# Kernel optimization log

Hardware: AMD Instinct MI355X
Metric: run time of the kernel (lower is better)

Reference implementation:

```python
import jax, jax.numpy as jnp
import numpy as np

N_NODES = 50000

def setup_inputs() -> dict:
    key = jax.random.key(0)
    k1, k2, k3, k4, k5 = jax.random.split(key, 5)
    feat = jax.random.normal(k1, (N_NODES, 192), dtype=jnp.float32)
    edge_feat = jax.random.normal(k2, (800000, 64), dtype=jnp.float32)
    src = jax.random.randint(k3, (800000,), 0, N_NODES, dtype=jnp.int32)
    dst = jax.random.randint(k4, (800000,), 0, N_NODES, dtype=jnp.int32)
    weight = jax.random.normal(k5, (256, 256), dtype=jnp.float32) * (1.0 / np.sqrt(256.0))
    bias = jnp.zeros((256,), dtype=jnp.float32)
    return {"feat": feat, "edge_feat": edge_feat, "src": src, "dst": dst,
            "weight": weight, "bias": bias}


def reference(feat, edge_feat, src, dst, weight, bias):
    N = feat.shape[0]
    ones_e = jnp.ones(src.shape[0], dtype=jnp.float32)
    # out-degree normalization of source features (pre-aggregation)
    out_deg = jnp.clip(jax.ops.segment_sum(ones_e, src, num_segments=N), 1.0, None)
    feat_n = feat * (out_deg ** -0.5)[:, None]            # [N, d_node]
    # message = concat(src_feat_norm, edge_feat); sum over dst.
    # segment_sum distributes over concat, so aggregate parts separately
    # (avoids materializing the [E, d_node+d_edge] message tensor).
    h_src = jax.ops.segment_sum(feat_n[src], dst, num_segments=N)   # [N, d_node]
    h_edge = jax.ops.segment_sum(edge_feat, dst, num_segments=N)    # [N, d_edge]
    h = jnp.concatenate([h_src, h_edge], axis=1)          # [N, in_feats]
    rst = h @ weight                                      # [N, out_feats]
    # in-degree normalization (post-aggregation)
    in_deg = jnp.clip(jax.ops.segment_sum(ones_e, dst, num_segments=N), 1.0, None)
    rst = rst * (in_deg ** -0.5)[:, None] + bias
    return rst
```

## Files before the change

kernel.cpp:

```cpp
#include <hip/hip_runtime.h>

#define NN 50000
#define NE 800000
#define DIN 256
#define DOUT 256


__global__ __launch_bounds__(256) void zero_meta(int* __restrict__ p, int n) {
    int i = blockIdx.x * 256 + threadIdx.x;
    if (i < n) p[i] = 0;
}

__global__ __launch_bounds__(256) void count_kernel(const int* __restrict__ src,
                                                    const int* __restrict__ dst,
                                                    int* __restrict__ in_cnt,
                                                    int* __restrict__ out_cnt) {
    int e = blockIdx.x * 256 + threadIdx.x;
    if (e < NE) {
        atomicAdd(in_cnt + dst[e], 1);
        atomicAdd(out_cnt + src[e], 1);
    }
}

__global__ __launch_bounds__(256) void scan1(const int* __restrict__ cnt,
                                             int* __restrict__ row_off,
                                             int* __restrict__ bsum) {
    __shared__ int tmp[256];
    int tid = threadIdx.x;
    int i = blockIdx.x * 256 + tid;
    int v = (i < NN) ? cnt[i] : 0;
    tmp[tid] = v;
    __syncthreads();
#pragma unroll
    for (int off = 1; off < 256; off <<= 1) {
        int t = (tid >= off) ? tmp[tid - off] : 0;
        __syncthreads();
        if (tid >= off) tmp[tid] += t;
        __syncthreads();
    }
    if (i < NN) row_off[i] = tmp[tid] - v;
    if (tid == 255) bsum[blockIdx.x] = tmp[255];
}

__global__ __launch_bounds__(256) void scan2(int* __restrict__ bsum, int nb) {
    __shared__ int tmp[256];
    int tid = threadIdx.x;
    int v = (tid < nb) ? bsum[tid] : 0;
    tmp[tid] = v;
    __syncthreads();
#pragma unroll
    for (int off = 1; off < 256; off <<= 1) {
        int t = (tid >= off) ? tmp[tid - off] : 0;
        __syncthreads();
        if (tid >= off) tmp[tid] += t;
        __syncthreads();
    }
    if (tid < nb) bsum[tid] = tmp[tid] - v;
}

__global__ __launch_bounds__(256) void scan3(int* __restrict__ row_off,
                                             int* __restrict__ cursor,
                                             const int* __restrict__ bsum) {
    int i = blockIdx.x * 256 + threadIdx.x;
    if (i < NN) {
        int v = row_off[i] + bsum[i >> 8];
        row_off[i] = v;
        cursor[i] = v;
    }
    if (i == NN) row_off[NN] = NE;
}

__global__ __launch_bounds__(256) void norm_out(const int* __restrict__ out_cnt,
                                                float* __restrict__ odeg_inv) {
    int i = blockIdx.x * 256 + threadIdx.x;
    if (i < NN) odeg_inv[i] = rsqrtf((float)max(out_cnt[i], 1));
}

__global__ __launch_bounds__(256) void fill_kernel(const int* __restrict__ src,
                                                   const int* __restrict__ dst,
                                                   int* __restrict__ cursor,
                                                   int2* __restrict__ perm2) {
    int e = blockIdx.x * 256 + threadIdx.x;
    if (e < NE) {
        int d = dst[e];
        int pos = atomicAdd(cursor + d, 1);
        perm2[pos] = make_int2(e, src[e]);
    }
}

__global__ __launch_bounds__(256) void aggregate_kernel(const float* __restrict__ feat,
                                                        const float* __restrict__ edge_feat,
                                                        const int* __restrict__ row_off,
                                                        const float* __restrict__ odeg_inv,
                                                        const int2* __restrict__ perm2,
                                                        float* __restrict__ h) {
    int node = blockIdx.x * 4 + (threadIdx.x >> 6);
    int lane = threadIdx.x & 63;
    if (node >= NN) return;
    int start = row_off[node];
    int end   = row_off[node + 1];

    bool isF = lane < 48;
    const float* base = isF ? feat : edge_feat;
    int stride = isF ? 192 : 64;
    int loff   = isF ? lane * 4 : (lane - 48) * 4;

    float4 acc = make_float4(0.f, 0.f, 0.f, 0.f);
    int i = start;
    for (; i + 4 <= end; i += 4) {
        int2 p0 = perm2[i + 0];
        int2 p1 = perm2[i + 1];
        int2 p2 = perm2[i + 2];
        int2 p3 = perm2[i + 3];
        int i0 = isF ? p0.y : p0.x;
        int i1 = isF ? p1.y : p1.x;
        int i2 = isF ? p2.y : p2.x;
        int i3 = isF ? p3.y : p3.x;
        float4 v0 = *(const float4*)(base + (size_t)i0 * stride + loff);
        float4 v1 = *(const float4*)(base + (size_t)i1 * stride + loff);
        float4 v2 = *(const float4*)(base + (size_t)i2 * stride + loff);
        float4 v3 = *(const float4*)(base + (size_t)i3 * stride + loff);
        float s0 = odeg_inv[p0.y]; if (!isF) s0 = 1.f;
        float s1 = odeg_inv[p1.y]; if (!isF) s1 = 1.f;
        float s2 = odeg_inv[p2.y]; if (!isF) s2 = 1.f;
        float s3 = odeg_inv[p3.y]; if (!isF) s3 = 1.f;
        acc.x = fmaf(v0.x, s0, acc.x); acc.y = fmaf(v0.y, s0, acc.y);
        acc.z = fmaf(v0.z, s0, acc.z); acc.w = fmaf(v0.w, s0, acc.w);
        acc.x = fmaf(v1.x, s1, acc.x); acc.y = fmaf(v1.y, s1, acc.y);
        acc.z = fmaf(v1.z, s1, acc.z); acc.w = fmaf(v1.w, s1, acc.w);
        acc.x = fmaf(v2.x, s2, acc.x); acc.y = fmaf(v2.y, s2, acc.y);
        acc.z = fmaf(v2.z, s2, acc.z); acc.w = fmaf(v2.w, s2, acc.w);
        acc.x = fmaf(v3.x, s3, acc.x); acc.y = fmaf(v3.y, s3, acc.y);
        acc.z = fmaf(v3.z, s3, acc.z); acc.w = fmaf(v3.w, s3, acc.w);
    }
    for (; i < end; ++i) {
        int2 p = perm2[i];
        int idx = isF ? p.y : p.x;
        float4 v = *(const float4*)(base + (size_t)idx * stride + loff);
        float s = odeg_inv[p.y]; if (!isF) s = 1.f;
        acc.x = fmaf(v.x, s, acc.x); acc.y = fmaf(v.y, s, acc.y);
        acc.z = fmaf(v.z, s, acc.z); acc.w = fmaf(v.w, s, acc.w);
    }
    ((float4*)h)[(size_t)node * 64 + lane] = acc;
}

#define HPAD 260
__global__ __launch_bounds__(256) void gemm_kernel(const float* __restrict__ h,
                                                   const float* __restrict__ W,
                                                   const float* __restrict__ bias,
                                                   const int* __restrict__ row_off,
                                                   float* __restrict__ out) {
    __shared__ float hs[32 * HPAD];
    int block_row = blockIdx.x * 32;

    for (int i = threadIdx.x; i < 32 * 64; i += 256) {
        int r = i >> 6, c4 = i & 63;
        int row = block_row + r;
        float4 v = make_float4(0.f, 0.f, 0.f, 0.f);
        if (row < NN) v = ((const float4*)h)[(size_t)row * 64 + c4];
        *(float4*)&hs[r * HPAD + c4 * 4] = v;
    }
    __syncthreads();

    int cg = threadIdx.x & 31;
    int rg = threadIdx.x >> 5;

    float acc[4][8];
#pragma unroll
    for (int i = 0; i < 4; ++i)
#pragma unroll
        for (int j = 0; j < 8; ++j) acc[i][j] = 0.f;

    const float4* W4 = (const float4*)W;
    for (int k4 = 0; k4 < 64; ++k4) {
        float4 a[4];
#pragma unroll
        for (int i = 0; i < 4; ++i)
            a[i] = *(const float4*)&hs[(rg * 4 + i) * HPAD + k4 * 4];
#pragma unroll
        for (int kk = 0; kk < 4; ++kk) {
            int k = k4 * 4 + kk;
            float4 w0 = W4[k * 64 + cg * 2];
            float4 w1 = W4[k * 64 + cg * 2 + 1];
#pragma unroll
            for (int i = 0; i < 4; ++i) {
                float av = ((const float*)&a[i])[kk];
                acc[i][0] = fmaf(av, w0.x, acc[i][0]);
                acc[i][1] = fmaf(av, w0.y, acc[i][1]);
                acc[i][2] = fmaf(av, w0.z, acc[i][2]);
                acc[i][3] = fmaf(av, w0.w, acc[i][3]);
                acc[i][4] = fmaf(av, w1.x, acc[i][4]);
                acc[i][5] = fmaf(av, w1.y, acc[i][5]);
                acc[i][6] = fmaf(av, w1.z, acc[i][6]);
                acc[i][7] = fmaf(av, w1.w, acc[i][7]);
            }
        }
    }

    float4 b0 = ((const float4*)bias)[cg * 2];
    float4 b1 = ((const float4*)bias)[cg * 2 + 1];
#pragma unroll
    for (int i = 0; i < 4; ++i) {
        int row = block_row + rg * 4 + i;
        if (row < NN) {
            int deg = row_off[row + 1] - row_off[row];
            float s = rsqrtf((float)max(deg, 1));
            float4 o0 = make_float4(acc[i][0] * s + b0.x, acc[i][1] * s + b0.y,
                                    acc[i][2] * s + b0.z, acc[i][3] * s + b0.w);
            float4 o1 = make_float4(acc[i][4] * s + b1.x, acc[i][5] * s + b1.y,
                                    acc[i][6] * s + b1.z, acc[i][7] * s + b1.w);
            float4* op = (float4*)(out + (size_t)row * DOUT + cg * 8);
            op[0] = o0;
            op[1] = o1;
        }
    }
}

extern "C" void kernel_launch(void* const* d_in, const int* in_sizes, int n_in,
                              void* d_out, int out_size, void* d_ws, size_t ws_size,
                              hipStream_t stream) {
    const float* feat      = (const float*)d_in[0];
    const float* edge_feat = (const float*)d_in[1];
    const int*   src       = (const int*)d_in[2];
    const int*   dst       = (const int*)d_in[3];
    const float* W         = (const float*)d_in[4];
    const float* bias      = (const float*)d_in[5];
    float* out = (float*)d_out;

    float* h        = (float*)d_ws;
    int*   row_off  = (int*)(h + (size_t)NN * DIN);
    float* odeg_inv = (float*)(row_off + NN + 2);
    int*   cursor   = (int*)(odeg_inv + NN);
    int*   bsum     = cursor + NN;
    int2*  perm2    = (int2*)(bsum + 256);
    int*   in_cnt   = (int*)perm2;
    int*   out_cnt  = in_cnt + NN;

    const int SCAN_BLOCKS = (NN + 255) / 256;

    zero_meta<<<(2 * NN + 255) / 256, 256, 0, stream>>>(in_cnt, 2 * NN);

    count_kernel<<<(NE + 255) / 256, 256, 0, stream>>>(src, dst, in_cnt, out_cnt);

    scan1<<<SCAN_BLOCKS, 256, 0, stream>>>(in_cnt, row_off, bsum);
    scan2<<<1, 256, 0, stream>>>(bsum, SCAN_BLOCKS);
    scan3<<<(NN + 256) / 256, 256, 0, stream>>>(row_off, cursor, bsum);

    norm_out<<<(NN + 255) / 256, 256, 0, stream>>>(out_cnt, odeg_inv);

    fill_kernel<<<(NE + 255) / 256, 256, 0, stream>>>(src, dst, cursor, perm2);

    aggregate_kernel<<<(NN + 3) / 4, 256, 0, stream>>>(feat, edge_feat, row_off,
                                                       odeg_inv, perm2, h);

    gemm_kernel<<<(NN + 31) / 32, 256, 0, stream>>>(h, W, bias, row_off, out);
}
```

Baseline: 615.9 us.

## Use bf16 MFMA GEMM, store aggregated features as bf16, widen gather unroll

Replaces the fp32 FMA GEMM with a bf16 MFMA 16x16x32 GEMM that reads a pre-transposed bf16 copy of the weight, converted by a new wconv kernel. The aggregation kernel now writes bf16 instead of fp32, halving the intermediate traffic, and gathers 8 edges per iteration with a clamped, masked tail instead of a 4-way unroll plus remainder loop. The out-degree normalisation is folded into scan3, so one launch disappears. The cost is lower precision in h and W (bf16 rounding), plus an extra launch for the weight conversion.

```diff
diff --git a/kernel.cpp b/kernel.cpp
--- a/kernel.cpp
+++ b/kernel.cpp
@@ -4,6 +4,15 @@
 #define NE 800000
 #define DIN 256
 #define DOUT 256
+
+typedef __attribute__((ext_vector_type(8))) short bf16x8;
+typedef __attribute__((ext_vector_type(4))) float f32x4;
+
+__device__ __forceinline__ unsigned short f2bf(float x) {
+    unsigned int u = __builtin_bit_cast(unsigned int, x);
+    u += 0x7fffu + ((u >> 16) & 1u);
+    return (unsigned short)(u >> 16);
+}
 
 
 __global__ __launch_bounds__(256) void zero_meta(int* __restrict__ p, int n) {
@@ -60,20 +69,23 @@
 
 __global__ __launch_bounds__(256) void scan3(int* __restrict__ row_off,
                                              int* __restrict__ cursor,
+                                             float* __restrict__ odeg_inv,
+                                             const int* __restrict__ out_cnt,
                                              const int* __restrict__ bsum) {
     int i = blockIdx.x * 256 + threadIdx.x;
     if (i < NN) {
         int v = row_off[i] + bsum[i >> 8];
         row_off[i] = v;
         cursor[i] = v;
+        odeg_inv[i] = rsqrtf((float)max(out_cnt[i], 1));
     }
     if (i == NN) row_off[NN] = NE;
 }
 
-__global__ __launch_bounds__(256) void norm_out(const int* __restrict__ out_cnt,
-                                                float* __restrict__ odeg_inv) {
-    int i = blockIdx.x * 256 + threadIdx.x;
-    if (i < NN) odeg_inv[i] = rsqrtf((float)max(out_cnt[i], 1));
+__global__ __launch_bounds__(256) void wconv(const float* __restrict__ W,
+                                             unsigned short* __restrict__ wt) {
+    int n = blockIdx.x, k = threadIdx.x;
+    wt[n * 256 + k] = f2bf(W[k * 256 + n]);
 }
 
 __global__ __launch_bounds__(256) void fill_kernel(const int* __restrict__ src,
@@ -93,7 +105,7 @@
                                                         const int* __restrict__ row_off,
                                                         const float* __restrict__ odeg_inv,
                                                         const int2* __restrict__ perm2,
-                                                        float* __restrict__ h) {
+                                                        unsigned short* __restrict__ h_bf) {
     int node = blockIdx.x * 4 + (threadIdx.x >> 6);
     int lane = threadIdx.x & 63;
     if (node >= NN) return;
@@ -106,113 +118,97 @@
     int loff   = isF ? lane * 4 : (lane - 48) * 4;
 
     float4 acc = make_float4(0.f, 0.f, 0.f, 0.f);
-    int i = start;
-    for (; i + 4 <= end; i += 4) {
-        int2 p0 = perm2[i + 0];
-        int2 p1 = perm2[i + 1];
-        int2 p2 = perm2[i + 2];
-        int2 p3 = perm2[i + 3];
-        int i0 = isF ? p0.y : p0.x;
-        int i1 = isF ? p1.y : p1.x;
-        int i2 = isF ? p2.y : p2.x;
-        int i3 = isF ? p3.y : p3.x;
-        float4 v0 = *(const float4*)(base + (size_t)i0 * stride + loff);
-        float4 v1 = *(const float4*)(base + (size_t)i1 * stride + loff);
-        float4 v2 = *(const float4*)(base + (size_t)i2 * stride + loff);
-        float4 v3 = *(const float4*)(base + (size_t)i3 * stride + loff);
-        float s0 = odeg_inv[p0.y]; if (!isF) s0 = 1.f;
-        float s1 = odeg_inv[p1.y]; if (!isF) s1 = 1.f;
-        float s2 = odeg_inv[p2.y]; if (!isF) s2 = 1.f;
-        float s3 = odeg_inv[p3.y]; if (!isF) s3 = 1.f;
-        acc.x = fmaf(v0.x, s0, acc.x); acc.y = fmaf(v0.y, s0, acc.y);
-        acc.z = fmaf(v0.z, s0, acc.z); acc.w = fmaf(v0.w, s0, acc.w);
-        acc.x = fmaf(v1.x, s1, acc.x); acc.y = fmaf(v1.y, s1, acc.y);
-        acc.z = fmaf(v1.z, s1, acc.z); acc.w = fmaf(v1.w, s1, acc.w);
-        acc.x = fmaf(v2.x, s2, acc.x); acc.y = fmaf(v2.y, s2, acc.y);
-        acc.z = fmaf(v2.z, s2, acc.z); acc.w = fmaf(v2.w, s2, acc.w);
-        acc.x = fmaf(v3.x, s3, acc.x); acc.y = fmaf(v3.y, s3, acc.y);
-        acc.z = fmaf(v3.z, s3, acc.z); acc.w = fmaf(v3.w, s3, acc.w);
-    }
-    for (; i < end; ++i) {
-        int2 p = perm2[i];
-        int idx = isF ? p.y : p.x;
-        float4 v = *(const float4*)(base + (size_t)idx * stride + loff);
-        float s = odeg_inv[p.y]; if (!isF) s = 1.f;
-        acc.x = fmaf(v.x, s, acc.x); acc.y = fmaf(v.y, s, acc.y);
-        acc.z = fmaf(v.z, s, acc.z); acc.w = fmaf(v.w, s, acc.w);
-    }
-    ((float4*)h)[(size_t)node * 64 + lane] = acc;
-}
-
-#define HPAD 260
-__global__ __launch_bounds__(256) void gemm_kernel(const float* __restrict__ h,
-                                                   const float* __restrict__ W,
-                                                   const float* __restrict__ bias,
-                                                   const int* __restrict__ row_off,
-                                                   float* __restrict__ out) {
-    __shared__ float hs[32 * HPAD];
-    int block_row = blockIdx.x * 32;
-
-    for (int i = threadIdx.x; i < 32 * 64; i += 256) {
-        int r = i >> 6, c4 = i & 63;
-        int row = block_row + r;
-        float4 v = make_float4(0.f, 0.f, 0.f, 0.f);
-        if (row < NN) v = ((const float4*)h)[(size_t)row * 64 + c4];
-        *(float4*)&hs[r * HPAD + c4 * 4] = v;
-    }
-    __syncthreads();
-
-    int cg = threadIdx.x & 31;
-    int rg = threadIdx.x >> 5;
-
-    float acc[4][8];
-#pragma unroll
-    for (int i = 0; i < 4; ++i)
-#pragma unroll
-        for (int j = 0; j < 8; ++j) acc[i][j] = 0.f;
-
-    const float4* W4 = (const float4*)W;
-    for (int k4 = 0; k4 < 64; ++k4) {
-        float4 a[4];
-#pragma unroll
-        for (int i = 0; i < 4; ++i)
-            a[i] = *(const float4*)&hs[(rg * 4 + i) * HPAD + k4 * 4];
-#pragma unroll
-        for (int kk = 0; kk < 4; ++kk) {
-            int k = k4 * 4 + kk;
-            float4 w0 = W4[k * 64 + cg * 2];
-            float4 w1 = W4[k * 64 + cg * 2 + 1];
-#pragma unroll
-            for (int i = 0; i < 4; ++i) {
-                float av = ((const float*)&a[i])[kk];
-                acc[i][0] = fmaf(av, w0.x, acc[i][0]);
-                acc[i][1] = fmaf(av, w0.y, acc[i][1]);
-                acc[i][2] = fmaf(av, w0.z, acc[i][2]);
-                acc[i][3] = fmaf(av, w0.w, acc[i][3]);
-                acc[i][4] = fmaf(av, w1.x, acc[i][4]);
-                acc[i][5] = fmaf(av, w1.y, acc[i][5]);
-                acc[i][6] = fmaf(av, w1.z, acc[i][6]);
-                acc[i][7] = fmaf(av, w1.w, acc[i][7]);
-            }
-        }
-    }
-
-    float4 b0 = ((const float4*)bias)[cg * 2];
-    float4 b1 = ((const float4*)bias)[cg * 2 + 1];
-#pragma unroll
-    for (int i = 0; i < 4; ++i) {
-        int row = block_row + rg * 4 + i;
-        if (row < NN) {
-            int deg = row_off[row + 1] - row_off[row];
-            float s = rsqrtf((float)max(deg, 1));
-            float4 o0 = make_float4(acc[i][0] * s + b0.x, acc[i][1] * s + b0.y,
-                                    acc[i][2] * s + b0.z, acc[i][3] * s + b0.w);
-            float4 o1 = make_float4(acc[i][4] * s + b1.x, acc[i][5] * s + b1.y,
-                                    acc[i][6] * s + b1.z, acc[i][7] * s + b1.w);
-            float4* op = (float4*)(out + (size_t)row * DOUT + cg * 8);
-            op[0] = o0;
-            op[1] = o1;
-        }
+    for (int i = start; i < end; i += 8) {
+        int2 p[8];
+        float4 v[8];
+        float w[8];
+#pragma unroll
+        for (int j = 0; j < 8; ++j) {
+            int ii = min(i + j, end - 1);
+            p[j] = perm2[ii];
+        }
+#pragma unroll
+        for (int j = 0; j < 8; ++j) {
+            int idx = isF ? p[j].y : p[j].x;
+            v[j] = *(const float4*)(base + (size_t)idx * stride + loff);
+        }
+#pragma unroll
+        for (int j = 0; j < 8; ++j) {
+            float s = isF ? odeg_inv[p[j].y] : 1.f;
+            w[j] = (i + j < end) ? s : 0.f;
+        }
+#pragma unroll
+        for (int j = 0; j < 8; ++j) {
+            acc.x = fmaf(v[j].x, w[j], acc.x);
+            acc.y = fmaf(v[j].y, w[j], acc.y);
+            acc.z = fmaf(v[j].z, w[j], acc.z);
+            acc.w = fmaf(v[j].w, w[j], acc.w);
+        }
+    }
+    ushort4 o;
+    o.x = f2bf(acc.x); o.y = f2bf(acc.y);
+    o.z = f2bf(acc.z); o.w = f2bf(acc.w);
+    *(ushort4*)(h_bf + (size_t)node * 256 + lane * 4) = o;
+}
+
+__global__ __launch_bounds__(256) void gemm_mfma(const unsigned short* __restrict__ h_bf,
+                                                 const unsigned short* __restrict__ wt_bf,
+                                                 const float* __restrict__ bias,
+                                                 const int* __restrict__ row_off,
+                                                 float* __restrict__ out) {
+    int wave = threadIdx.x >> 6;
+    int lane = threadIdx.x & 63;
+    int m16  = lane & 15;
+    int quad = lane >> 4;
+    int rbase = blockIdx.x * 16;
+    int cbase = wave * 64;
+
+    const unsigned short* arow = h_bf + (size_t)(rbase + m16) * 256 + quad * 8;
+    const unsigned short* b0p = wt_bf + (size_t)(cbase +  0 + m16) * 256 + quad * 8;
+    const unsigned short* b1p = wt_bf + (size_t)(cbase + 16 + m16) * 256 + quad * 8;
+    const unsigned short* b2p = wt_bf + (size_t)(cbase + 32 + m16) * 256 + quad * 8;
+    const unsigned short* b3p = wt_bf + (size_t)(cbase + 48 + m16) * 256 + quad * 8;
+
+    f32x4 acc0 = {0.f, 0.f, 0.f, 0.f};
+    f32x4 acc1 = {0.f, 0.f, 0.f, 0.f};
+    f32x4 acc2 = {0.f, 0.f, 0.f, 0.f};
+    f32x4 acc3 = {0.f, 0.f, 0.f, 0.f};
+
+#pragma unroll
+    for (int k0 = 0; k0 < 256; k0 += 32) {
+        bf16x8 a  = *(const bf16x8*)(arow + k0);
+        bf16x8 b0 = *(const bf16x8*)(b0p + k0);
+        bf16x8 b1 = *(const bf16x8*)(b1p + k0);
+        bf16x8 b2 = *(const bf16x8*)(b2p + k0);
+        bf16x8 b3 = *(const bf16x8*)(b3p + k0);
+        acc0 = __builtin_amdgcn_mfma_f32_16x16x32_bf16(a, b0, acc0, 0, 0, 0);
+        acc1 = __builtin_amdgcn_mfma_f32_16x16x32_bf16(a, b1, acc1, 0, 0, 0);
+        acc2 = __builtin_amdgcn_mfma_f32_16x16x32_bf16(a, b2, acc2, 0, 0, 0);
+        acc3 = __builtin_amdgcn_mfma_f32_16x16x32_bf16(a, b3, acc3, 0, 0, 0);
+    }
+
+    int grow0 = rbase + quad * 4;
+    float s[4];
+    int ro_prev = row_off[grow0];
+#pragma unroll
+    for (int r = 0; r < 4; ++r) {
+        int nx = row_off[grow0 + r + 1];
+        s[r] = rsqrtf((float)max(nx - ro_prev, 1));
+        ro_prev = nx;
+    }
+
+    float bv0 = bias[cbase +  0 + m16];
+    float bv1 = bias[cbase + 16 + m16];
+    float bv2 = bias[cbase + 32 + m16];
+    float bv3 = bias[cbase + 48 + m16];
+
+#pragma unroll
+    for (int r = 0; r < 4; ++r) {
+        size_t rowoff = (size_t)(grow0 + r) * DOUT;
+        out[rowoff + cbase +  0 + m16] = acc0[r] * s[r] + bv0;
+        out[rowoff + cbase + 16 + m16] = acc1[r] * s[r] + bv1;
+        out[rowoff + cbase + 32 + m16] = acc2[r] * s[r] + bv2;
+        out[rowoff + cbase + 48 + m16] = acc3[r] * s[r] + bv3;
     }
 }
 
@@ -227,8 +223,9 @@
     const float* bias      = (const float*)d_in[5];
     float* out = (float*)d_out;
 
-    float* h        = (float*)d_ws;
-    int*   row_off  = (int*)(h + (size_t)NN * DIN);
+    unsigned short* h_bf    = (unsigned short*)d_ws;
+    unsigned short* wt_bf   = h_bf + (size_t)NN * DIN;
+    int*   row_off  = (int*)(wt_bf + 256 * 256);
     float* odeg_inv = (float*)(row_off + NN + 2);
     int*   cursor   = (int*)(odeg_inv + NN);
     int*   bsum     = cursor + NN;
@@ -239,19 +236,13 @@
     const int SCAN_BLOCKS = (NN + 255) / 256;
 
     zero_meta<<<(2 * NN + 255) / 256, 256, 0, stream>>>(in_cnt, 2 * NN);
-
     count_kernel<<<(NE + 255) / 256, 256, 0, stream>>>(src, dst, in_cnt, out_cnt);
-
     scan1<<<SCAN_BLOCKS, 256, 0, stream>>>(in_cnt, row_off, bsum);
     scan2<<<1, 256, 0, stream>>>(bsum, SCAN_BLOCKS);
-    scan3<<<(NN + 256) / 256, 256, 0, stream>>>(row_off, cursor, bsum);
-
-    norm_out<<<(NN + 255) / 256, 256, 0, stream>>>(out_cnt, odeg_inv);
-
+    scan3<<<(NN + 256) / 256, 256, 0, stream>>>(row_off, cursor, odeg_inv, out_cnt, bsum);
+    wconv<<<256, 256, 0, stream>>>(W, wt_bf);
     fill_kernel<<<(NE + 255) / 256, 256, 0, stream>>>(src, dst, cursor, perm2);
-
     aggregate_kernel<<<(NN + 3) / 4, 256, 0, stream>>>(feat, edge_feat, row_off,
-                                                       odeg_inv, perm2, h);
-
-    gemm_kernel<<<(NN + 31) / 32, 256, 0, stream>>>(h, W, bias, row_off, out);
-}
+                                                       odeg_inv, perm2, h_bf);
+    gemm_mfma<<<NN / 16, 256, 0, stream>>>(h_bf, wt_bf, bias, row_off, out);
+}
```

Result: faster. 564.0 us (-8.4%).
